# Performance work log

Measured on AMD Instinct MI355X. Metric: run time of the kernel, lower is better.

Reference implementation:

```python
import jax, jax.numpy as jnp
import numpy as np

N = 20000
E = 320000
F_IN = 50
HID = 64          # hidden_channels
HEADS = 8
WIDTH = HID * HEADS  # 512
NUM_CLASSES = 121


def setup_inputs() -> dict:
    key = jax.random.key(0)
    ks = jax.random.split(key, 16)
    def p(k, shape, fan_in):
        return (jax.random.normal(k, shape, dtype=jnp.float32) / np.sqrt(fan_in)).astype(jnp.float32)
    x = jax.random.normal(ks[0], (N, F_IN), dtype=jnp.float32)
    edge_index = jax.random.randint(ks[1], (2, E), 0, N, dtype=jnp.int64)
    return {
        "x": x,
        "edge_index": edge_index,
        # layer 1: 50 -> 64, heads=8, concat
        "W1": p(ks[2], (F_IN, HEADS * HID), F_IN),
        "a1_src": p(ks[3], (HEADS, HID), HID),
        "a1_dst": p(ks[4], (HEADS, HID), HID),
        "b1": jnp.zeros((HEADS * HID,), jnp.float32),
        # layer 2: 512 -> 512, heads=1, concat
        "W2": p(ks[5], (WIDTH, WIDTH), WIDTH),
        "a2_src": p(ks[6], (1, WIDTH), WIDTH),
        "a2_dst": p(ks[7], (1, WIDTH), WIDTH),
        "b2": jnp.zeros((WIDTH,), jnp.float32),
        # layer 3: 512 -> 121, heads=1, concat=False (mean)
        "W3": p(ks[8], (WIDTH, NUM_CLASSES), WIDTH),
        "a3_src": p(ks[9], (1, NUM_CLASSES), NUM_CLASSES),
        "a3_dst": p(ks[10], (1, NUM_CLASSES), NUM_CLASSES),
        "b3": jnp.zeros((NUM_CLASSES,), jnp.float32),
    }


def gat_conv(x, src, dst, W, a_src, a_dst, b, heads, out_ch, concat):
    n = x.shape[0]
    h = (x @ W).reshape(n, heads, out_ch)                 # [N, H, C]
    al_s = jnp.sum(h * a_src, axis=-1)                     # [N, H]
    al_d = jnp.sum(h * a_dst, axis=-1)                     # [N, H]
    e = jax.nn.leaky_relu(al_s[src] + al_d[dst], 0.2)      # [E, H]
    # edge softmax per destination node (stable)
    m = jax.ops.segment_max(e, dst, num_segments=n)        # [N, H]
    m = jnp.where(jnp.isfinite(m), m, 0.0)
    ex = jnp.exp(e - m[dst])
    z = jax.ops.segment_sum(ex, dst, num_segments=n)       # [N, H]
    alpha = ex / (z[dst] + 1e-16)                          # [E, H]
    msg = h[src] * alpha[..., None]                        # [E, H, C]
    out = jax.ops.segment_sum(msg, dst, num_segments=n)    # [N, H, C]
    out = out.reshape(n, heads * out_ch) if concat else out.mean(axis=1)
    return out + b


def reference(x, edge_index, W1, a1_src, a1_dst, b1, W2, a2_src, a2_dst, b2, W3, a3_src, a3_dst, b3):
    n = x.shape[0]
    # PyG GATConv adds self loops by default
    loops = jnp.arange(n, dtype=edge_index.dtype)
    src = jnp.concatenate([edge_index[0], loops])
    dst = jnp.concatenate([edge_index[1], loops])
    # eval mode: dropout is identity
    x1 = gat_conv(x, src, dst, W1, a1_src, a1_dst, b1, HEADS, HID, True)
    h = jax.nn.elu(x1)
    x1 = gat_conv(h, src, dst, W2, a2_src, a2_dst, b2, 1, WIDTH, True)
    h = jax.nn.elu(x1)
    x1 = gat_conv(h, src, dst, W3, a3_src, a3_dst, b3, 1, NUM_CLASSES, False)
    return x1
```

## Files before the change

### kernel.cpp

```cpp
#include <hip/hip_runtime.h>
#include <hip/hip_bf16.h>
#include <hip/hip_fp16.h>

#define NN     20000
#define ERAW   320000
#define ETOT   (ERAW + NN)
#define F_IN   50
#define HID    64
#define HEADS  8
#define WIDTH  512
#define NCLS   121
#define NCLS_P 128

typedef __attribute__((ext_vector_type(8))) __bf16 bf16x8;
typedef __attribute__((ext_vector_type(4))) float floatx4;

__device__ __forceinline__ unsigned short f32_to_bf16_rn(float f) {
  unsigned u = __float_as_uint(f);
  unsigned r = u + 0x7fffu + ((u >> 16) & 1u);
  return (unsigned short)(r >> 16);
}
__device__ __forceinline__ void split_one(float f, unsigned short& h,
                                          unsigned short& l) {
  h = f32_to_bf16_rn(f);
  float fh = __uint_as_float(((unsigned)h) << 16);
  l = f32_to_bf16_rn(f - fh);
}

__device__ __forceinline__ float2 u2f2(unsigned u) {
  __half2 hv = *reinterpret_cast<__half2*>(&u);
  return __half22float2(hv);
}

__global__ __launch_bounds__(256) void transpose_split(
    const float* __restrict__ W, unsigned short* __restrict__ thi,
    unsigned short* __restrict__ tlo, int K, int M, int Mp) {
  __shared__ float t[32][33];
  int k0 = blockIdx.x * 32, m0 = blockIdx.y * 32;
  int tx = threadIdx.x & 31, ty = threadIdx.x >> 5;
  #pragma unroll
  for (int r = 0; r < 4; ++r) {
    int k = k0 + ty + r * 8, m = m0 + tx;
    float v = 0.f;
    if (k < K && m < M) v = W[(size_t)k * M + m];
    t[ty + r * 8][tx] = v;
  }
  __syncthreads();
  #pragma unroll
  for (int r = 0; r < 4; ++r) {
    int m = m0 + ty + r * 8, k = k0 + tx;
    if (m < Mp && k < K) {
      unsigned short h, l;
      split_one(t[tx][ty + r * 8], h, l);
      thi[(size_t)m * K + k] = h;
      tlo[(size_t)m * K + k] = l;
    }
  }
}

__global__ __launch_bounds__(256) void build_w1h_t(
    const float* __restrict__ W1, unsigned short* __restrict__ thi,
    unsigned short* __restrict__ tlo) {
  int idx = blockIdx.x * blockDim.x + threadIdx.x;
  if (idx >= HEADS * HID * HID) return;
  int hd = idx >> 12, rem = idx & 4095;
  int col = rem >> 6, k = rem & 63;
  float v = (k < F_IN) ? W1[(size_t)k * WIDTH + hd * HID + col] : 0.f;
  unsigned short h, l;
  split_one(v, h, l);
  thi[idx] = h;
  tlo[idx] = l;
}

__global__ __launch_bounds__(256) void gemm_mfma_split(
    const unsigned short* __restrict__ Ahi, const unsigned short* __restrict__ Alo,
    const unsigned short* __restrict__ Bthi, const unsigned short* __restrict__ Btlo,
    float* __restrict__ C, __half* __restrict__ C16, int N, int K, int M) {
  __shared__ unsigned short sAhi[4096], sAlo[4096], sBhi[4096], sBlo[4096];
  const int tid = threadIdx.x;
  const int wave = tid >> 6, lane = tid & 63;
  const int wr = wave >> 1, wc = wave & 1;
  const int r0 = blockIdx.y * 128;
  const int c0 = blockIdx.x * 128;
  const int lkg = lane >> 4;
  const int lmn = lane & 15;

  const int skg = tid & 3;
  const int srow = tid >> 2;
  int ra0 = r0 + srow;        if (ra0 > NN - 1) ra0 = NN - 1;
  int ra1 = r0 + srow + 64;   if (ra1 > NN - 1) ra1 = NN - 1;
  const unsigned short* gAhi0 = Ahi + (size_t)ra0 * K + skg * 8;
  const unsigned short* gAhi1 = Ahi + (size_t)ra1 * K + skg * 8;
  const unsigned short* gAlo0 = Alo + (size_t)ra0 * K + skg * 8;
  const unsigned short* gAlo1 = Alo + (size_t)ra1 * K + skg * 8;
  const unsigned short* gBhi0 = Bthi + (size_t)(c0 + srow) * K + skg * 8;
  const unsigned short* gBhi1 = Bthi + (size_t)(c0 + srow + 64) * K + skg * 8;
  const unsigned short* gBlo0 = Btlo + (size_t)(c0 + srow) * K + skg * 8;
  const unsigned short* gBlo1 = Btlo + (size_t)(c0 + srow + 64) * K + skg * 8;

  floatx4 acc[4][4] = {};

  uint4 a0, a1, a2, a3, b0, b1, b2, b3;
  auto gload = [&](int kk) {
    a0 = *(const uint4*)(gAhi0 + kk);
    a1 = *(const uint4*)(gAhi1 + kk);
    a2 = *(const uint4*)(gAlo0 + kk);
    a3 = *(const uint4*)(gAlo1 + kk);
    b0 = *(const uint4*)(gBhi0 + kk);
    b1 = *(const uint4*)(gBhi1 + kk);
    b2 = *(const uint4*)(gBlo0 + kk);
    b3 = *(const uint4*)(gBlo1 + kk);
  };
  gload(0);

  const int w0 = (skg * 128 + srow) * 8;
  const int w1 = (skg * 128 + srow + 64) * 8;

  for (int k0 = 0; k0 < K; k0 += 32) {
    __syncthreads();
    *(uint4*)(sAhi + w0) = a0;
    *(uint4*)(sAhi + w1) = a1;
    *(uint4*)(sAlo + w0) = a2;
    *(uint4*)(sAlo + w1) = a3;
    *(uint4*)(sBhi + w0) = b0;
    *(uint4*)(sBhi + w1) = b1;
    *(uint4*)(sBlo + w0) = b2;
    *(uint4*)(sBlo + w1) = b3;
    __syncthreads();
    if (k0 + 32 < K) gload(k0 + 32);

    bf16x8 fAhi[4], fAlo[4], fBhi[4], fBlo[4];
    #pragma unroll
    for (int mi = 0; mi < 4; ++mi) {
      int m = wr * 64 + mi * 16 + lmn;
      fAhi[mi] = *(const bf16x8*)(sAhi + (lkg * 128 + m) * 8);
      fAlo[mi] = *(const bf16x8*)(sAlo + (lkg * 128 + m) * 8);
    }
    #pragma unroll
    for (int ni = 0; ni < 4; ++ni) {
      int n = wc * 64 + ni * 16 + lmn;
      fBhi[ni] = *(const bf16x8*)(sBhi + (lkg * 128 + n) * 8);
      fBlo[ni] = *(const bf16x8*)(sBlo + (lkg * 128 + n) * 8);
    }
    #pragma unroll
    for (int mi = 0; mi < 4; ++mi)
      #pragma unroll
      for (int ni = 0; ni < 4; ++ni) {
        acc[mi][ni] = __builtin_amdgcn_mfma_f32_16x16x32_bf16(
            fAhi[mi], fBhi[ni], acc[mi][ni], 0, 0, 0);
        acc[mi][ni] = __builtin_amdgcn_mfma_f32_16x16x32_bf16(
            fAhi[mi], fBlo[ni], acc[mi][ni], 0, 0, 0);
        acc[mi][ni] = __builtin_amdgcn_mfma_f32_16x16x32_bf16(
            fAlo[mi], fBhi[ni], acc[mi][ni], 0, 0, 0);
      }
  }

  #pragma unroll
  for (int mi = 0; mi < 4; ++mi) {
    #pragma unroll
    for (int r = 0; r < 4; ++r) {
      int grow = r0 + wr * 64 + mi * 16 + (lane >> 4) * 4 + r;
      if (grow >= N) continue;
      #pragma unroll
      for (int ni = 0; ni < 4; ++ni) {
        int gcol = c0 + wc * 64 + ni * 16 + lmn;
        if (gcol < M) {
          float v = acc[mi][ni][r];
          C[(size_t)grow * M + gcol] = v;
          C16[(size_t)grow * M + gcol] = __float2half(v);
        }
      }
    }
  }
}

__global__ __launch_bounds__(256) void gemm_l1_heads(
    const unsigned short* __restrict__ Ahi, const unsigned short* __restrict__ Alo,
    const unsigned short* __restrict__ Bthi, const unsigned short* __restrict__ Btlo,
    unsigned short* __restrict__ outHi, unsigned short* __restrict__ outLo,
    const float* __restrict__ bias) {
  __shared__ unsigned short sAhi[8192], sAlo[8192], sBhi[4096], sBlo[4096];
  const int tid = threadIdx.x;
  const int wave = tid >> 6, lane = tid & 63;
  const int r0 = blockIdx.x * 128;
  const int hd = blockIdx.y;
  const int lkg = lane >> 4, lmn = lane & 15;

  #pragma unroll
  for (int t = 0; t < 4; ++t) {
    int cid = tid + t * 256;
    int row = cid >> 3, c = cid & 7;
    int gr = r0 + row; if (gr > NN - 1) gr = NN - 1;
    const size_t goff = (size_t)gr * WIDTH + hd * HID + c * 8;
    int loff = (((c >> 2) * 4 + (c & 3)) * 128 + row) * 8;
    *(uint4*)(sAhi + loff) = *(const uint4*)(Ahi + goff);
    *(uint4*)(sAlo + loff) = *(const uint4*)(Alo + goff);
  }
  #pragma unroll
  for (int t = 0; t < 2; ++t) {
    int cid = tid + t * 256;
    int col = cid >> 3, c = cid & 7;
    const size_t goff = (size_t)(hd * HID + col) * HID + c * 8;
    int loff = (((c >> 2) * 4 + (c & 3)) * 64 + col) * 8;
    *(uint4*)(sBhi + loff) = *(const uint4*)(Bthi + goff);
    *(uint4*)(sBlo + loff) = *(const uint4*)(Btlo + goff);
  }
  __syncthreads();

  floatx4 acc[2][4] = {};
  #pragma unroll
  for (int ks = 0; ks < 2; ++ks) {
    bf16x8 fAhi[2], fAlo[2], fBhi[4], fBlo[4];
    #pragma unroll
    for (int mi = 0; mi < 2; ++mi) {
      int m = wave * 32 + mi * 16 + lmn;
      int off = ((ks * 4 + lkg) * 128 + m) * 8;
      fAhi[mi] = *(const bf16x8*)(sAhi + off);
      fAlo[mi] = *(const bf16x8*)(sAlo + off);
    }
    #pragma unroll
    for (int ni = 0; ni < 4; ++ni) {
      int n = ni * 16 + lmn;
      int off = ((ks * 4 + lkg) * 64 + n) * 8;
      fBhi[ni] = *(const bf16x8*)(sBhi + off);
      fBlo[ni] = *(const bf16x8*)(sBlo + off);
    }
    #pragma unroll
    for (int mi = 0; mi < 2; ++mi)
      #pragma unroll
      for (int ni = 0; ni < 4; ++ni) {
        acc[mi][ni] = __builtin_amdgcn_mfma_f32_16x16x32_bf16(
            fAhi[mi], fBhi[ni], acc[mi][ni], 0, 0, 0);
        acc[mi][ni] = __builtin_amdgcn_mfma_f32_16x16x32_bf16(
            fAhi[mi], fBlo[ni], acc[mi][ni], 0, 0, 0);
        acc[mi][ni] = __builtin_amdgcn_mfma_f32_16x16x32_bf16(
            fAlo[mi], fBhi[ni], acc[mi][ni], 0, 0, 0);
      }
  }

  #pragma unroll
  for (int mi = 0; mi < 2; ++mi) {
    #pragma unroll
    for (int r = 0; r < 4; ++r) {
      int grow = r0 + wave * 32 + mi * 16 + (lane >> 4) * 4 + r;
      if (grow >= NN) continue;
      #pragma unroll
      for (int ni = 0; ni < 4; ++ni) {
        int gcol = hd * HID + ni * 16 + lmn;
        float v = acc[mi][ni][r] + bias[gcol];
        v = (v > 0.f) ? v : (__expf(v) - 1.0f);
        unsigned short hh, ll;
        split_one(v, hh, ll);
        outHi[(size_t)grow * WIDTH + gcol] = hh;
        outLo[(size_t)grow * WIDTH + gcol] = ll;
      }
    }
  }
}

__global__ __launch_bounds__(256) void fold_w1a(
    const float* __restrict__ W1, const float* __restrict__ a1s,
    const float* __restrict__ a1d, float* __restrict__ w1as,
    float* __restrict__ w1ad) {
  int idx = blockIdx.x * blockDim.x + threadIdx.x;
  if (idx >= 2 * F_IN * HEADS) return;
  int which = idx >= F_IN * HEADS;
  int r = which ? idx - F_IN * HEADS : idx;
  int k = r >> 3, h = r & 7;
  const float* a = which ? a1d : a1s;
  float s = 0.f;
  for (int c = 0; c < HID; ++c) s += W1[(size_t)k * WIDTH + h * HID + c] * a[h * HID + c];
  (which ? w1ad : w1as)[r] = s;
}

__global__ __launch_bounds__(256) void al1_kernel(
    const float* __restrict__ x, const float* __restrict__ w1as,
    const float* __restrict__ w1ad, float* __restrict__ al_s,
    float* __restrict__ al_d) {
  int n = (blockIdx.x * blockDim.x + threadIdx.x) >> 6;
  int lane = threadIdx.x & 63;
  if (n >= NN) return;
  float xv = (lane < F_IN) ? x[(size_t)n * F_IN + lane] : 0.f;
  float ws[HEADS], wd[HEADS];
  #pragma unroll
  for (int h = 0; h < HEADS; ++h) {
    ws[h] = (lane < F_IN) ? w1as[lane * HEADS + h] : 0.f;
    wd[h] = (lane < F_IN) ? w1ad[lane * HEADS + h] : 0.f;
  }
  #pragma unroll
  for (int h = 0; h < HEADS; ++h) {
    float ss = xv * ws[h], sd = xv * wd[h];
    #pragma unroll
    for (int o = 32; o; o >>= 1) {
      ss += __shfl_xor(ss, o);
      sd += __shfl_xor(sd, o);
    }
    if (lane == 0) {
      al_s[n * HEADS + h] = ss;
      al_d[n * HEADS + h] = sd;
    }
  }
}

__global__ __launch_bounds__(256) void compute_al(
    const float* __restrict__ h, const float* __restrict__ a_src,
    const float* __restrict__ a_dst, float* __restrict__ al_s,
    float* __restrict__ al_d, int Nn, int H, int C) {
  int wave = (blockIdx.x * blockDim.x + threadIdx.x) >> 6;
  int lane = threadIdx.x & 63;
  if (wave >= Nn) return;
  const float* hr = h + (size_t)wave * H * C;
  for (int hd = 0; hd < H; ++hd) {
    float ss = 0.f, sd = 0.f;
    for (int c = lane; c < C; c += 64) {
      float v = hr[hd * C + c];
      ss += v * a_src[hd * C + c];
      sd += v * a_dst[hd * C + c];
    }
    #pragma unroll
    for (int o = 32; o; o >>= 1) {
      ss += __shfl_xor(ss, o);
      sd += __shfl_xor(sd, o);
    }
    if (lane == 0) {
      al_s[wave * H + hd] = ss;
      al_d[wave * H + hd] = sd;
    }
  }
}

__global__ __launch_bounds__(256) void count_deg(
    const int* __restrict__ edst, int* __restrict__ deg) {
  int e = blockIdx.x * blockDim.x + threadIdx.x;
  if (e >= ETOT) return;
  int d = (e < ERAW) ? edst[e] : (e - ERAW);
  atomicAdd(&deg[d], 1);
}

__global__ __launch_bounds__(256) void scan_deg(
    const int* __restrict__ deg, int* __restrict__ rowptr) {
  __shared__ int part[256];
  const int t = threadIdx.x;
  const int CHUNK = (NN + 255) / 256;
  int lo = t * CHUNK, hi = min(lo + CHUNK, NN);
  int s = 0;
  for (int i = lo; i < hi; ++i) s += deg[i];
  part[t] = s;
  __syncthreads();
  for (int off = 1; off < 256; off <<= 1) {
    int v = (t >= off) ? part[t - off] : 0;
    __syncthreads();
    part[t] += v;
    __syncthreads();
  }
  int base = (t == 0) ? 0 : part[t - 1];
  for (int i = lo; i < hi; ++i) {
    rowptr[i] = base;
    base += deg[i];
  }
  if (t == 255) rowptr[NN] = part[255];
}

__global__ __launch_bounds__(256) void scatter_csr(
    const int* __restrict__ esrc, const int* __restrict__ edst,
    const int* __restrict__ rowptr, int* __restrict__ cnt,
    int* __restrict__ csrc) {
  int e = blockIdx.x * blockDim.x + threadIdx.x;
  if (e >= ETOT) return;
  int s, d;
  if (e < ERAW) { s = esrc[e]; d = edst[e]; }
  else          { s = e - ERAW; d = e - ERAW; }
  int pos = rowptr[d] + atomicAdd(&cnt[d], 1);
  csrc[pos] = s;
}

__global__ __launch_bounds__(256) void agg_x_sm(
    const int* __restrict__ rowptr, const int* __restrict__ csrc,
    const float* __restrict__ al_s, const float* __restrict__ al_d,
    const float* __restrict__ x, unsigned short* __restrict__ outHi,
    unsigned short* __restrict__ outLo) {
  const int w = threadIdx.x >> 6, lane = threadIdx.x & 63;
  const int d = blockIdx.x * 4 + w;
  if (d >= NN) return;
  const int r0 = rowptr[d], r1 = rowptr[d + 1];
  const int mh = lane & 7;
  const float ald_my = al_d[d * HEADS + mh];
  float m_my = al_s[d * HEADS + mh] + ald_my;
  m_my = (m_my > 0.f) ? m_my : 0.2f * m_my;

  float z_my = 0.f;
  float acc[HEADS];
  #pragma unroll
  for (int hh = 0; hh < HEADS; ++hh) acc[hh] = 0.f;
  for (int p = r0; p < r1; ++p) {
    int s = csrc[p];
    float v = al_s[s * HEADS + mh] + ald_my;
    v = (v > 0.f) ? v : 0.2f * v;
    float a = __expf(v - m_my);
    z_my += a;
    float xv = (lane < F_IN) ? x[(size_t)s * F_IN + lane] : 0.f;
    #pragma unroll
    for (int hh = 0; hh < HEADS; ++hh) acc[hh] += __shfl(a, hh, 8) * xv;
  }
  #pragma unroll
  for (int hh = 0; hh < HEADS; ++hh) {
    float zh = __shfl(z_my, hh, 8);
    float v = (lane < F_IN) ? acc[hh] / (zh + 1e-16f) : 0.f;
    unsigned short h2, l2;
    split_one(v, h2, l2);
    outHi[(size_t)d * WIDTH + hh * HID + lane] = h2;
    outLo[(size_t)d * WIDTH + hh * HID + lane] = l2;
  }
}

template <int M, bool ELU, bool SPLIT>
__global__ __launch_bounds__(256) void pull_agg_sm(
    const int* __restrict__ rowptr, const int* __restrict__ csrc,
    const float* __restrict__ al_s, const float* __restrict__ al_d,
    const __half* __restrict__ h16, const float* __restrict__ bias,
    float* __restrict__ out, unsigned short* __restrict__ outHi,
    unsigned short* __restrict__ outLo) {
  constexpr int EPL = (M + 63) / 64;
  const int w = threadIdx.x >> 6;
  const int lane = threadIdx.x & 63;
  const int d = blockIdx.x * 4 + w;
  if (d >= NN) return;
  const int r0 = rowptr[d], r1 = rowptr[d + 1];
  const float ald = al_d[d];
  float m = al_s[d] + ald;
  m = (m > 0.f) ? m : 0.2f * m;

  const int base = lane * EPL;
  float acc[EPL];
  #pragma unroll
  for (int j = 0; j < EPL; ++j) acc[j] = 0.f;
  float z = 0.f;

  for (int p = r0; p < r1; ++p) {
    int s = csrc[p];
    float v = al_s[s] + ald;
    v = (v > 0.f) ? v : 0.2f * v;
    float a = __expf(v - m);
    z += a;
    const __half* hr = h16 + (size_t)s * M + base;
    if (M % 64 == 0 && EPL == 8) {
      uint4 raw = *(const uint4*)hr;
      float2 f0 = u2f2(raw.x), f1 = u2f2(raw.y);
      float2 f2 = u2f2(raw.z), f3 = u2f2(raw.w);
      acc[0] += f0.x * a; acc[1] += f0.y * a;
      acc[2] += f1.x * a; acc[3] += f1.y * a;
      acc[4] += f2.x * a; acc[5] += f2.y * a;
      acc[6] += f3.x * a; acc[7] += f3.y * a;
    } else {
      #pragma unroll
      for (int j = 0; j < EPL; ++j) {
        if ((M % 64 == 0) || (base + j < M))
          acc[j] += __half2float(hr[j]) * a;
      }
    }
  }
  const float iz = 1.0f / (z + 1e-16f);

  #pragma unroll
  for (int j = 0; j < EPL; ++j) {
    if ((M % 64 == 0) || (base + j < M)) {
      float v = acc[j] * iz + bias[base + j];
      if (ELU) v = (v > 0.f) ? v : (__expf(v) - 1.0f);
      if (SPLIT) {
        unsigned short hh, ll;
        split_one(v, hh, ll);
        outHi[(size_t)d * M + base + j] = hh;
        outLo[(size_t)d * M + base + j] = ll;
      } else {
        out[(size_t)d * M + base + j] = v;
      }
    }
  }
}

extern "C" void kernel_launch(void* const* d_in, const int* in_sizes, int n_in,
                              void* d_out, int out_size, void* d_ws,
                              size_t ws_size, hipStream_t stream) {
  const float* x      = (const float*)d_in[0];
  const int*   ei     = (const int*)d_in[1];
  const float* W1     = (const float*)d_in[2];
  const float* a1_src = (const float*)d_in[3];
  const float* a1_dst = (const float*)d_in[4];
  const float* b1     = (const float*)d_in[5];
  const float* W2     = (const float*)d_in[6];
  const float* a2_src = (const float*)d_in[7];
  const float* a2_dst = (const float*)d_in[8];
  const float* b2     = (const float*)d_in[9];
  const float* W3     = (const float*)d_in[10];
  const float* a3_src = (const float*)d_in[11];
  const float* a3_dst = (const float*)d_in[12];
  const float* b3     = (const float*)d_in[13];
  float* out = (float*)d_out;

  const int* esrc = ei;
  const int* edst = ei + ERAW;

  unsigned short* p1Hi  = (unsigned short*)d_ws;
  unsigned short* p1Lo  = p1Hi + (size_t)NN * WIDTH;
  unsigned short* p2Hi  = p1Lo + (size_t)NN * WIDTH;
  unsigned short* p2Lo  = p2Hi + (size_t)NN * WIDTH;
  __half*        h16    = (__half*)(p2Lo + (size_t)NN * WIDTH);
  unsigned short* w1hHi = (unsigned short*)(h16 + (size_t)NN * WIDTH);
  unsigned short* w1hLo = w1hHi + (size_t)HEADS * HID * HID;
  unsigned short* w2tHi = w1hLo + (size_t)HEADS * HID * HID;
  unsigned short* w2tLo = w2tHi + (size_t)WIDTH * WIDTH;
  unsigned short* w3tHi = w2tLo + (size_t)WIDTH * WIDTH;
  unsigned short* w3tLo = w3tHi + (size_t)NCLS_P * WIDTH;
  float* bufA   = (float*)(w3tLo + (size_t)NCLS_P * WIDTH);
  float* al_s   = bufA + (size_t)NN * WIDTH;
  float* al_d   = al_s + (size_t)NN * HEADS;
  float* w1as   = al_d + (size_t)NN * HEADS;
  float* w1ad   = w1as + F_IN * HEADS;
  int* deg      = (int*)(w1ad + F_IN * HEADS);
  int* rowptr   = deg + NN;
  int* cnt      = rowptr + NN + 4;
  int* csrc     = cnt + NN;

  hipMemsetAsync(deg, 0, (size_t)NN * sizeof(int), stream);
  hipMemsetAsync(cnt, 0, (size_t)NN * sizeof(int), stream);
  const int eblk = (ETOT + 255) / 256;
  count_deg<<<eblk, 256, 0, stream>>>(edst, deg);
  scan_deg<<<1, 256, 0, stream>>>(deg, rowptr);
  scatter_csr<<<eblk, 256, 0, stream>>>(esrc, edst, rowptr, cnt, csrc);

  build_w1h_t<<<(HEADS * HID * HID + 255) / 256, 256, 0, stream>>>(W1, w1hHi,
                                                                   w1hLo);
  transpose_split<<<dim3(WIDTH / 32, WIDTH / 32), 256, 0, stream>>>(
      W2, w2tHi, w2tLo, WIDTH, WIDTH, WIDTH);
  transpose_split<<<dim3(WIDTH / 32, NCLS_P / 32), 256, 0, stream>>>(
      W3, w3tHi, w3tLo, WIDTH, NCLS, NCLS_P);

  const int nwblk = (NN + 3) / 4;

  {
    fold_w1a<<<(2 * F_IN * HEADS + 255) / 256, 256, 0, stream>>>(
        W1, a1_src, a1_dst, w1as, w1ad);
    al1_kernel<<<nwblk, 256, 0, stream>>>(x, w1as, w1ad, al_s, al_d);
    agg_x_sm<<<nwblk, 256, 0, stream>>>(rowptr, csrc, al_s, al_d, x, p1Hi,
                                        p1Lo);
    gemm_l1_heads<<<dim3((NN + 127) / 128, HEADS), 256, 0, stream>>>(
        p1Hi, p1Lo, w1hHi, w1hLo, p2Hi, p2Lo, b1);
  }
  {
    gemm_mfma_split<<<dim3(WIDTH / 128, (NN + 127) / 128), 256, 0, stream>>>(
        p2Hi, p2Lo, w2tHi, w2tLo, bufA, h16, NN, WIDTH, WIDTH);
    compute_al<<<nwblk, 256, 0, stream>>>(bufA, a2_src, a2_dst, al_s, al_d,
                                          NN, 1, WIDTH);
    pull_agg_sm<WIDTH, true, true><<<nwblk, 256, 0, stream>>>(
        rowptr, csrc, al_s, al_d, h16, b2, nullptr, p1Hi, p1Lo);
  }
  {
    gemm_mfma_split<<<dim3(NCLS_P / 128, (NN + 127) / 128), 256, 0, stream>>>(
        p1Hi, p1Lo, w3tHi, w3tLo, bufA, h16, NN, WIDTH, NCLS);
    compute_al<<<nwblk, 256, 0, stream>>>(bufA, a3_src, a3_dst, al_s, al_d,
                                          NN, 1, NCLS);
    pull_agg_sm<NCLS, false, false><<<nwblk, 256, 0, stream>>>(
        rowptr, csrc, al_s, al_d, h16, b3, out, nullptr, nullptr);
  }
}
```

Baseline: 482.4 us.

## Pre-bucket edges by source before CSR scatter to sort neighbor lists

Adds a first counting-sort pass that groups edges by source node and then builds the destination CSR from that source-ordered list. Because edges are scattered in source order, each destination's neighbor list ends up roughly sorted by source, which should give better cache locality when the aggregation kernels gather source rows. It adds a histogram, a scan and a scatter pass plus extra memsets and buffers, and the one-block scan runs serially. Atomic ordering within a destination is still nondeterministic, so the sort is only approximate.

```diff
diff --git a/kernel.cpp b/kernel.cpp
--- a/kernel.cpp
+++ b/kernel.cpp
@@ -327,6 +327,20 @@
       al_d[wave * H + hd] = sd;
     }
   }
+}
+
+__device__ __forceinline__ void edge_sd2(int e, const int* esrc,
+                                         const int* edst, int& s, int& d) {
+  if (e < ERAW) { s = esrc[e]; d = edst[e]; }
+  else          { s = e - ERAW; d = e - ERAW; }
+}
+
+__global__ __launch_bounds__(256) void count_src(
+    const int* __restrict__ esrc, int* __restrict__ hist) {
+  int e = blockIdx.x * blockDim.x + threadIdx.x;
+  if (e >= ETOT) return;
+  int s = (e < ERAW) ? esrc[e] : (e - ERAW);
+  atomicAdd(&hist[s], 1);
 }
 
 __global__ __launch_bounds__(256) void count_deg(
@@ -361,17 +375,28 @@
   if (t == 255) rowptr[NN] = part[255];
 }
 
-__global__ __launch_bounds__(256) void scatter_csr(
+__global__ __launch_bounds__(256) void scatter_by_src(
     const int* __restrict__ esrc, const int* __restrict__ edst,
-    const int* __restrict__ rowptr, int* __restrict__ cnt,
-    int* __restrict__ csrc) {
+    const int* __restrict__ srcptr, int* __restrict__ cnt_s,
+    int* __restrict__ es_src, int* __restrict__ es_dst) {
   int e = blockIdx.x * blockDim.x + threadIdx.x;
   if (e >= ETOT) return;
   int s, d;
-  if (e < ERAW) { s = esrc[e]; d = edst[e]; }
-  else          { s = e - ERAW; d = e - ERAW; }
+  edge_sd2(e, esrc, edst, s, d);
+  int pos = srcptr[s] + atomicAdd(&cnt_s[s], 1);
+  es_src[pos] = s;
+  es_dst[pos] = d;
+}
+
+__global__ __launch_bounds__(256) void scatter_csr_sorted(
+    const int* __restrict__ es_src, const int* __restrict__ es_dst,
+    const int* __restrict__ rowptr, int* __restrict__ cnt,
+    int* __restrict__ csrc) {
+  int p = blockIdx.x * blockDim.x + threadIdx.x;
+  if (p >= ETOT) return;
+  int d = es_dst[p];
   int pos = rowptr[d] + atomicAdd(&cnt[d], 1);
-  csrc[pos] = s;
+  csrc[pos] = es_src[p];
 }
 
 __global__ __launch_bounds__(256) void agg_x_sm(
@@ -519,14 +544,26 @@
   int* deg      = (int*)(w1ad + F_IN * HEADS);
   int* rowptr   = deg + NN;
   int* cnt      = rowptr + NN + 4;
-  int* csrc     = cnt + NN;
+  int* hist_s   = cnt + NN;
+  int* srcptr   = hist_s + NN;
+  int* cnt_s    = srcptr + NN + 4;
+  int* csrc     = cnt_s + NN;
+  int* es_src   = csrc + ETOT;
+  int* es_dst   = es_src + ETOT;
 
   hipMemsetAsync(deg, 0, (size_t)NN * sizeof(int), stream);
   hipMemsetAsync(cnt, 0, (size_t)NN * sizeof(int), stream);
+  hipMemsetAsync(hist_s, 0, (size_t)NN * sizeof(int), stream);
+  hipMemsetAsync(cnt_s, 0, (size_t)NN * sizeof(int), stream);
   const int eblk = (ETOT + 255) / 256;
+  count_src<<<eblk, 256, 0, stream>>>(esrc, hist_s);
+  scan_deg<<<1, 256, 0, stream>>>(hist_s, srcptr);
+  scatter_by_src<<<eblk, 256, 0, stream>>>(esrc, edst, srcptr, cnt_s,
+                                           es_src, es_dst);
   count_deg<<<eblk, 256, 0, stream>>>(edst, deg);
   scan_deg<<<1, 256, 0, stream>>>(deg, rowptr);
-  scatter_csr<<<eblk, 256, 0, stream>>>(esrc, edst, rowptr, cnt, csrc);
+  scatter_csr_sorted<<<eblk, 256, 0, stream>>>(es_src, es_dst, rowptr, cnt,
+                                               csrc);
 
   build_w1h_t<<<(HEADS * HID * HID + 255) / 256, 256, 0, stream>>>(W1, w1hHi,
                                                                    w1hLo);
```

New measurement: 556.2 us. +15.3%, slower.
